# Kernel tuning notes

Hardware: AMD Instinct MI355X
Metric: run time of the kernel (lower is better)

Reference implementation:

```python
import jax, jax.numpy as jnp
import numpy as np

B, C, H, W = 16, 256, 32, 32
NH, DH = 16, 16          # n_heads, n_head_channels; NH*DH == C
STRIDE, KK = 2, 9        # offset conv stride / kernel (stage_idx=0)
Hk, Wk = 16, 16          # offset map size = H/stride
NS = Hk * Wk             # n_sample
EPS_LN, EPS_BN = 1e-5, 1e-5


def conv1x1(x, w, b=None):
    # x: [B,Ci,H,W], w: [Co,Ci]
    y = jnp.einsum('bihw,oi->bohw', x, w)
    if b is not None:
        y = y + b[None, :, None, None]
    return y


def dwconv(x, w, b):
    # depthwise conv, w: [C,1,KK,KK]
    y = jax.lax.conv_general_dilated(
        x, w, (STRIDE, STRIDE), [(KK // 2, KK // 2)] * 2,
        dimension_numbers=('NCHW', 'OIHW', 'NCHW'),
        feature_group_count=x.shape[1])
    return y + b[None, :, None, None]


def ln_channels(x, g, b):
    # LayerNormProxy: layer-norm over channel dim of NCHW
    m = jnp.mean(x, axis=1, keepdims=True)
    v = jnp.mean((x - m) ** 2, axis=1, keepdims=True)
    return (x - m) / jnp.sqrt(v + EPS_LN) * g[None, :, None, None] + b[None, :, None, None]


def ref_points(hk, wk, b):
    # normalized (y, x) reference grid in [-1, 1], matching _get_ref_points
    ry = (jnp.arange(hk, dtype=jnp.float32) + 0.5) / hk * 2.0 - 1.0
    rx = (jnp.arange(wk, dtype=jnp.float32) + 0.5) / wk * 2.0 - 1.0
    ref = jnp.stack(jnp.meshgrid(ry, rx, indexing='ij'), axis=-1)  # [hk,wk,2] (y,x)
    return jnp.broadcast_to(ref[None], (b, hk, wk, 2))


def grid_sample_bilinear(img, grid):
    # img: [B,C,H,W]; grid: [B,Hg,Wg,2] in (x,y) order, [-1,1], align_corners=True,
    # zeros padding (matches torch F.grid_sample defaults).
    Bi, Ci, Hi, Wi = img.shape
    gx = (grid[..., 0] + 1.0) * 0.5 * (Wi - 1)
    gy = (grid[..., 1] + 1.0) * 0.5 * (Hi - 1)
    x0 = jnp.floor(gx); y0 = jnp.floor(gy)
    x1 = x0 + 1.0;      y1 = y0 + 1.0
    wx1 = gx - x0; wx0 = 1.0 - wx1
    wy1 = gy - y0; wy0 = 1.0 - wy1
    imgf = img.reshape(Bi, Ci, Hi * Wi)

    def gather(yi, xi):
        valid = (yi >= 0) & (yi < Hi) & (xi >= 0) & (xi < Wi)
        idx = (jnp.clip(yi, 0, Hi - 1) * Wi + jnp.clip(xi, 0, Wi - 1)).astype(jnp.int32)
        v = jnp.take_along_axis(imgf, idx.reshape(Bi, 1, -1), axis=2)  # [B,C,Hg*Wg]
        return v * valid.reshape(Bi, 1, -1).astype(img.dtype)

    out = (gather(y0, x0) * (wy0 * wx0).reshape(Bi, 1, -1)
           + gather(y0, x1) * (wy0 * wx1).reshape(Bi, 1, -1)
           + gather(y1, x0) * (wy1 * wx0).reshape(Bi, 1, -1)
           + gather(y1, x1) * (wy1 * wx1).reshape(Bi, 1, -1))
    return out.reshape(Bi, Ci, grid.shape[1], grid.shape[2])


def setup_inputs() -> dict:
    key = jax.random.key(0)
    ks = jax.random.split(key, 16)
    s = 0.05
    return {
        'x':        jax.random.normal(ks[0], (B, C, H, W), jnp.float32),
        'wq':       jax.random.normal(ks[1], (C, C), jnp.float32) * s,
        'bq':       jax.random.normal(ks[2], (C,), jnp.float32) * s,
        'off_dw_w': jax.random.normal(ks[3], (C, 1, KK, KK), jnp.float32) * s,
        'off_dw_b': jax.random.normal(ks[4], (C,), jnp.float32) * s,
        'ln_g':     jnp.ones((C,), jnp.float32),
        'ln_b':     jnp.zeros((C,), jnp.float32),
        'off_pw_w': jax.random.normal(ks[5], (2, C), jnp.float32) * s,
        'wk':       jax.random.normal(ks[6], (C, C), jnp.float32) * s,
        'bk':       jax.random.normal(ks[7], (C,), jnp.float32) * s,
        'wv':       jax.random.normal(ks[8], (C, C), jnp.float32) * s,
        'bv':       jax.random.normal(ks[9], (C,), jnp.float32) * s,
        'wo':       jax.random.normal(ks[10], (C, C), jnp.float32) * s,
        'bo':       jax.random.normal(ks[11], (C,), jnp.float32) * s,
        'bn_g':     jnp.ones((C,), jnp.float32),
        'bn_b':     jnp.zeros((C,), jnp.float32),
        'bn_m':     jax.random.normal(ks[12], (C,), jnp.float32) * s,
        'bn_v':     jax.random.uniform(ks[13], (C,), jnp.float32) + 0.5,
    }


def reference(x, wq, bq, off_dw_w, off_dw_b, ln_g, ln_b, off_pw_w,
              wk, bk, wv, bv, wo, bo, bn_g, bn_b, bn_m, bn_v):
    q = conv1x1(x, wq, bq)                                 # [B,C,H,W]
    # offset branch (n_groups=1 so q_off == q)
    off = dwconv(q, off_dw_w, off_dw_b)                    # [B,C,Hk,Wk]
    off = jax.nn.gelu(ln_channels(off, ln_g, ln_b), approximate=False)
    offset = jnp.einsum('bihw,oi->bohw', off, off_pw_w)    # [B,2,Hk,Wk] (y,x)
    offset = jnp.transpose(offset, (0, 2, 3, 1))           # [B,Hk,Wk,2]
    ref = ref_points(Hk, Wk, B)
    pos = jnp.tanh(offset + ref)                           # offset_range_factor[0] < 0 branch
    # deformable sampling: grid takes (x,y)
    xs = grid_sample_bilinear(x, pos[..., ::-1])           # [B,C,Hk,Wk]
    xs = xs.reshape(B, C, 1, NS)
    k = conv1x1(xs, wk, bk).reshape(B * NH, DH, NS)
    v = conv1x1(xs, wv, bv).reshape(B * NH, DH, NS)
    qf = q.reshape(B * NH, DH, H * W)
    attn = jnp.einsum('bcm,bcn->bmn', qf, k) * (DH ** -0.5)  # [B*NH, H*W, NS]
    attn = jax.nn.softmax(attn, axis=2)
    out = jnp.einsum('bmn,bcn->bcm', attn, v).reshape(B, C, H, W)
    y = conv1x1(out, wo, bo)
    # BatchNorm2d in eval mode with running stats
    y = ((y - bn_m[None, :, None, None]) / jnp.sqrt(bn_v[None, :, None, None] + EPS_BN)
         * bn_g[None, :, None, None] + bn_b[None, :, None, None])
    return y
```

## Files before the change

kernel.cpp:

```cpp
#include <hip/hip_runtime.h>
#include <hip/hip_bf16.h>
#include <math.h>

#define BATCH 16
#define CH    256
#define HW    1024
#define NS    256
#define NH    16
#define DH    16

typedef __attribute__((ext_vector_type(8))) short short8v;
typedef __attribute__((ext_vector_type(4))) float float4v;

__device__ __forceinline__ unsigned short f2bf(float f) {
    union { float f; unsigned u; } v; v.f = f;
    unsigned r = v.u + 0x7FFFu + ((v.u >> 16) & 1u);
    return (unsigned short)(r >> 16);
}

__global__ __launch_bounds__(256) void prep_k(
    const float* __restrict__ wq, const float* __restrict__ wk,
    const float* __restrict__ wv, const float* __restrict__ wo,
    unsigned short* __restrict__ Wf,
    const float* __restrict__ x, unsigned short* __restrict__ xT)
{
    int blk = blockIdx.x;
    if (blk < 1024) {
        const float* W;
        switch (blk >> 8) {
            case 0: W = wq; break;
            case 1: W = wk; break;
            case 2: W = wv; break;
            default: W = wo; break;
        }
        int e = (blk & 255) * 256 + threadIdx.x;
        int i = e & 7, l = (e >> 3) & 63, kt = (e >> 9) & 7, ot = e >> 12;
        float v = W[(ot * 16 + (l & 15)) * 256 + kt * 32 + 8 * (l >> 4) + i];
        Wf[(blk >> 8) * 65536 + e] = f2bf(v);
    } else {
        int xb = blk - 1024;
        int b = xb >> 4, pblk = (xb >> 2) & 3, cblk = xb & 3;
        int p = pblk * 256 + threadIdx.x;
        const float* xp = x + (size_t)b * CH * HW + p;
        unsigned short* o = xT + ((size_t)b * HW + p) * CH;
        #pragma unroll
        for (int cc = 0; cc < 64; cc += 8) {
            int c0 = cblk * 64 + cc;
            short8v t;
            #pragma unroll
            for (int i = 0; i < 8; ++i) t[i] = (short)f2bf(xp[(size_t)(c0 + i) * HW]);
            *(short8v*)&o[c0] = t;
        }
    }
}

template<int P, int MODE>
__global__ __launch_bounds__(256) void gemm_k(
    const unsigned short* __restrict__ Wf, const unsigned short* __restrict__ XT,
    const float* __restrict__ bias, const float* __restrict__ bias2,
    float* __restrict__ outF, unsigned short* __restrict__ outB,
    unsigned short* __restrict__ outB2,
    const float* __restrict__ bn_g, const float* __restrict__ bn_b,
    const float* __restrict__ bn_m, const float* __restrict__ bn_v)
{
    const int bz  = blockIdx.z;
    const int b   = (MODE == 1) ? (bz & 15) : bz;
    const int mat = (MODE == 1) ? (bz >> 4) : 0;
    const unsigned short* Wfm = Wf + mat * 65536;

    const int t = threadIdx.x, lane = t & 63, wvi = t >> 6;
    const int g = lane >> 4, col = lane & 15;
    const int o0 = blockIdx.x * 64;
    const int p0 = blockIdx.y * 128 + wvi * 32;
    const unsigned short* xb = XT + ((size_t)b * P + p0) * CH;

    float4v acc[4][2];
    #pragma unroll
    for (int mi = 0; mi < 4; ++mi)
        #pragma unroll
        for (int ni = 0; ni < 2; ++ni) {
            float4v z = {0.f, 0.f, 0.f, 0.f};
            acc[mi][ni] = z;
        }

    #pragma unroll
    for (int kt = 0; kt < 8; ++kt) {
        short8v af[4], bf[2];
        #pragma unroll
        for (int mi = 0; mi < 4; ++mi)
            af[mi] = *(const short8v*)&Wfm[(((((o0 >> 4) + mi) * 8) + kt) * 64 + lane) * 8];
        #pragma unroll
        for (int ni = 0; ni < 2; ++ni)
            bf[ni] = *(const short8v*)&xb[(size_t)(ni * 16 + col) * CH + kt * 32 + 8 * g];
        #pragma unroll
        for (int mi = 0; mi < 4; ++mi)
            #pragma unroll
            for (int ni = 0; ni < 2; ++ni)
                acc[mi][ni] = __builtin_amdgcn_mfma_f32_16x16x32_bf16(
                    af[mi], bf[ni], acc[mi][ni], 0, 0, 0);
    }

    const float* bp = (MODE == 1 && mat == 1) ? bias2 : bias;
    #pragma unroll
    for (int mi = 0; mi < 4; ++mi) {
        const int ob = o0 + mi * 16 + 4 * g;
        float bs[4];
        #pragma unroll
        for (int ii = 0; ii < 4; ++ii) bs[ii] = bp[ob + ii];

        if (MODE == 2) {
            float sc[4], sh[4];
            #pragma unroll
            for (int ii = 0; ii < 4; ++ii) {
                int o = ob + ii;
                float s = bn_g[o] * rsqrtf(bn_v[o] + 1e-5f);
                sc[ii] = s;
                sh[ii] = bn_b[o] - bn_m[o] * s + bs[ii] * s;
            }
            #pragma unroll
            for (int ni = 0; ni < 2; ++ni) {
                int p = p0 + ni * 16 + col;
                #pragma unroll
                for (int ii = 0; ii < 4; ++ii)
                    outF[((size_t)(b * CH + ob + ii)) * P + p] =
                        acc[mi][ni][ii] * sc[ii] + sh[ii];
            }
        } else {
            #pragma unroll
            for (int ni = 0; ni < 2; ++ni) {
                int p = p0 + ni * 16 + col;
                float v0 = acc[mi][ni][0] + bs[0];
                float v1 = acc[mi][ni][1] + bs[1];
                float v2 = acc[mi][ni][2] + bs[2];
                float v3 = acc[mi][ni][3] + bs[3];
                if (MODE == 0) {
                    outF[((size_t)(b * CH + ob + 0)) * P + p] = v0;
                    outF[((size_t)(b * CH + ob + 1)) * P + p] = v1;
                    outF[((size_t)(b * CH + ob + 2)) * P + p] = v2;
                    outF[((size_t)(b * CH + ob + 3)) * P + p] = v3;
                    uint2 w;
                    w.x = (unsigned)f2bf(v0) | ((unsigned)f2bf(v1) << 16);
                    w.y = (unsigned)f2bf(v2) | ((unsigned)f2bf(v3) << 16);
                    *(uint2*)&outB[((size_t)(b * P + p)) * CH + ob] = w;
                } else {
                    if (mat == 0) {
                        uint2 w;
                        w.x = (unsigned)f2bf(v0) | ((unsigned)f2bf(v1) << 16);
                        w.y = (unsigned)f2bf(v2) | ((unsigned)f2bf(v3) << 16);
                        *(uint2*)&outB[((size_t)(b * P + p)) * CH + ob] = w;
                    } else {
                        outB2[((size_t)(b * CH + ob + 0)) * P + p] = f2bf(v0);
                        outB2[((size_t)(b * CH + ob + 1)) * P + p] = f2bf(v1);
                        outB2[((size_t)(b * CH + ob + 2)) * P + p] = f2bf(v2);
                        outB2[((size_t)(b * CH + ob + 3)) * P + p] = f2bf(v3);
                    }
                }
            }
        }
    }
}

__global__ __launch_bounds__(256) void dwconv_k(
    const float* __restrict__ q, const float* __restrict__ w,
    const float* __restrict__ bias, float* __restrict__ off)
{
    int bc = blockIdx.x;
    int c  = bc & (CH - 1);
    __shared__ float plane[HW];
    __shared__ float kw[81];
    int t = threadIdx.x;
    const float* qp = q + (size_t)bc * HW;
    #pragma unroll
    for (int j = t; j < HW; j += 256) plane[j] = qp[j];
    if (t < 81) kw[t] = w[c * 81 + t];
    __syncthreads();
    int hk = t >> 4, wk = t & 15;
    float s = bias[c];
    int yb = hk * 2 - 4, xb = wk * 2 - 4;
    #pragma unroll
    for (int dy = 0; dy < 9; ++dy) {
        int yy = yb + dy;
        if ((unsigned)yy < 32u) {
            #pragma unroll
            for (int dx = 0; dx < 9; ++dx) {
                int xx = xb + dx;
                if ((unsigned)xx < 32u) s += kw[dy * 9 + dx] * plane[yy * 32 + xx];
            }
        }
    }
    off[(size_t)bc * NS + t] = s;
}

__device__ inline void block_reduce2(float& a, float& b, int t, float* sbuf)
{
    #pragma unroll
    for (int o = 32; o > 0; o >>= 1) {
        a += __shfl_down(a, o);
        b += __shfl_down(b, o);
    }
    int w = t >> 6;
    if ((t & 63) == 0) { sbuf[w * 2] = a; sbuf[w * 2 + 1] = b; }
    __syncthreads();
    a = sbuf[0] + sbuf[2] + sbuf[4] + sbuf[6];
    b = sbuf[1] + sbuf[3] + sbuf[5] + sbuf[7];
    __syncthreads();
}

__global__ __launch_bounds__(256) void lngs_k(
    const float* __restrict__ off, const float* __restrict__ ln_g,
    const float* __restrict__ ln_b, const float* __restrict__ pw,
    const float* __restrict__ x, unsigned short* __restrict__ xsT)
{
    __shared__ float sbuf[8];
    int bs = blockIdx.x;
    int b = bs >> 8, s = bs & 255;
    int c = threadIdx.x;
    float v = off[((size_t)(b * CH + c)) * NS + s];
    float a = v, q2 = v * v;
    block_reduce2(a, q2, c, sbuf);
    float mean = a * (1.0f / 256.0f);
    float var  = q2 * (1.0f / 256.0f) - mean * mean;
    float xn = (v - mean) * rsqrtf(var + 1e-5f) * ln_g[c] + ln_b[c];
    float g = 0.5f * xn * (1.0f + erff(xn * 0.70710678118654752f));
    float d0 = g * pw[c];
    float d1 = g * pw[CH + c];
    block_reduce2(d0, d1, c, sbuf);

    int hk = s >> 4, wk = s & 15;
    float ry = ((hk + 0.5f) / 16.0f) * 2.0f - 1.0f;
    float rx = ((wk + 0.5f) / 16.0f) * 2.0f - 1.0f;
    float py = tanhf(d0 + ry);
    float px = tanhf(d1 + rx);

    float gx = (px + 1.0f) * 0.5f * 31.0f;
    float gy = (py + 1.0f) * 0.5f * 31.0f;
    float x0f = floorf(gx), y0f = floorf(gy);
    int ix = (int)x0f, iy = (int)y0f;
    float wx1 = gx - x0f, wx0 = 1.0f - wx1;
    float wy1 = gy - y0f, wy0 = 1.0f - wy1;
    const float* img = x + ((size_t)b * CH + c) * HW;
    float v00 = ((unsigned)iy < 32u && (unsigned)ix < 32u) ? img[iy * 32 + ix] : 0.0f;
    float v01 = ((unsigned)iy < 32u && (unsigned)(ix + 1) < 32u) ? img[iy * 32 + ix + 1] : 0.0f;
    float v10 = ((unsigned)(iy + 1) < 32u && (unsigned)ix < 32u) ? img[(iy + 1) * 32 + ix] : 0.0f;
    float v11 = ((unsigned)(iy + 1) < 32u && (unsigned)(ix + 1) < 32u) ? img[(iy + 1) * 32 + ix + 1] : 0.0f;
    float vv = wy0 * wx0 * v00 + wy0 * wx1 * v01 + wy1 * wx0 * v10 + wy1 * wx1 * v11;
    xsT[(size_t)bs * CH + c] = f2bf(vv);
}

__global__ __launch_bounds__(256) void attn_mfma_k(
    const unsigned short* __restrict__ qT, const unsigned short* __restrict__ kT,
    const unsigned short* __restrict__ vbf, unsigned short* __restrict__ aoT)
{
    const int bh   = blockIdx.x >> 2;
    const int mseg = blockIdx.x & 3;
    const int b = bh >> 4, h = bh & 15;

    __shared__ short Kp[16 * 64 * 8];
    __shared__ short Vsh[16 * 256];
    __shared__ short Ps[4][16 * 32];

    const int tid  = threadIdx.x;
    const int lane = tid & 63;
    const int wvi  = tid >> 6;
    const int col  = lane & 15;
    const int g    = lane >> 4;

    for (int e = tid; e < 512; e += 256) {
        int t = e >> 5, l = e & 31, gg = l >> 4, c = l & 15;
        short8v kk = *(const short8v*)&kT[((size_t)(b * NS + 16 * t + c)) * CH + h * 16 + 8 * gg];
        *(short8v*)&Kp[(t * 64 + l) * 8] = kk;
        short8v z = {0, 0, 0, 0, 0, 0, 0, 0};
        *(short8v*)&Kp[(t * 64 + 32 + l) * 8] = z;
    }
    {
        const unsigned short* Vb = vbf + ((size_t)(b * CH + h * 16)) * NS;
        int d = tid >> 4, n0 = (tid & 15) * 16;
        char* vb = (char*)Vsh;
        #pragma unroll
        for (int hh = 0; hh < 2; ++hh) {
            short8v pk = *(const short8v*)&Vb[(size_t)d * NS + n0 + 8 * hh];
            *(short8v*)(vb + ((d * 512 + (n0 + 8 * hh) * 2) ^ ((d & 7) << 4))) = pk;
        }
    }
    __syncthreads();

    const unsigned short* Qb = qT + (size_t)b * HW * CH + h * 16;
    unsigned short*       Ob = aoT + (size_t)b * HW * CH + h * 16;
    char* pbase = (char*)Ps[wvi];
    char* vbase = (char*)Vsh;

    for (int mt = 0; mt < 4; ++mt) {
        const int m0 = mseg * 256 + wvi * 64 + mt * 16;

        short8v qf = {0, 0, 0, 0, 0, 0, 0, 0};
        if (g < 2)
            qf = *(const short8v*)&Qb[(size_t)(m0 + col) * CH + 8 * g];

        float4v p[16];
        #pragma unroll
        for (int t = 0; t < 16; ++t) {
            short8v kf = *(const short8v*)&Kp[(t * 64 + lane) * 8];
            float4v z = {0.f, 0.f, 0.f, 0.f};
            p[t] = __builtin_amdgcn_mfma_f32_16x16x32_bf16(kf, qf, z, 0, 0, 0);
        }

        float mx = -1e30f;
        #pragma unroll
        for (int t = 0; t < 16; ++t)
            mx = fmaxf(mx, fmaxf(fmaxf(p[t][0], p[t][1]), fmaxf(p[t][2], p[t][3])));
        mx = fmaxf(mx, __shfl_xor(mx, 16));
        mx = fmaxf(mx, __shfl_xor(mx, 32));
        float sum = 0.f;
        #pragma unroll
        for (int t = 0; t < 16; ++t) {
            #pragma unroll
            for (int i = 0; i < 4; ++i) {
                float e = __expf((p[t][i] - mx) * 0.25f);
                p[t][i] = e;
                sum += e;
            }
        }
        sum += __shfl_xor(sum, 16);
        sum += __shfl_xor(sum, 32);
        const float inv = 1.0f / sum;

        float4v acc = {0.f, 0.f, 0.f, 0.f};
        #pragma unroll
        for (int c = 0; c < 8; ++c) {
            #pragma unroll
            for (int pp = 0; pp < 2; ++pp) {
                float4v pv = p[2 * c + pp];
                uint2 wr;
                wr.x = (unsigned)f2bf(pv[0]) | ((unsigned)f2bf(pv[1]) << 16);
                wr.y = (unsigned)f2bf(pv[2]) | ((unsigned)f2bf(pv[3]) << 16);
                *(uint2*)(pbase + ((col * 64 + (16 * pp + 4 * g) * 2) ^ ((col & 7) << 4))) = wr;
            }
            short8v pf = *(const short8v*)(pbase + ((col * 64 + 16 * g) ^ ((col & 7) << 4)));
            short8v vf = *(const short8v*)(vbase + ((col * 512 + 64 * c + 16 * g) ^ ((col & 7) << 4)));
            acc = __builtin_amdgcn_mfma_f32_16x16x32_bf16(vf, pf, acc, 0, 0, 0);
        }

        uint2 w;
        w.x = (unsigned)f2bf(acc[0] * inv) | ((unsigned)f2bf(acc[1] * inv) << 16);
        w.y = (unsigned)f2bf(acc[2] * inv) | ((unsigned)f2bf(acc[3] * inv) << 16);
        *(uint2*)&Ob[(size_t)(m0 + col) * CH + 4 * g] = w;
    }
}

extern "C" void kernel_launch(void* const* d_in, const int* in_sizes, int n_in,
                              void* d_out, int out_size, void* d_ws, size_t ws_size,
                              hipStream_t stream)
{
    const float* x        = (const float*)d_in[0];
    const float* wq       = (const float*)d_in[1];
    const float* bq       = (const float*)d_in[2];
    const float* off_dw_w = (const float*)d_in[3];
    const float* off_dw_b = (const float*)d_in[4];
    const float* ln_g     = (const float*)d_in[5];
    const float* ln_b     = (const float*)d_in[6];
    const float* off_pw_w = (const float*)d_in[7];
    const float* wk       = (const float*)d_in[8];
    const float* bk       = (const float*)d_in[9];
    const float* wv       = (const float*)d_in[10];
    const float* bv       = (const float*)d_in[11];
    const float* wo       = (const float*)d_in[12];
    const float* bo       = (const float*)d_in[13];
    const float* bn_g     = (const float*)d_in[14];
    const float* bn_b     = (const float*)d_in[15];
    const float* bn_m     = (const float*)d_in[16];
    const float* bn_v     = (const float*)d_in[17];

    float* ws  = (float*)d_ws;
    float* q   = ws;
    float* off = q + 4194304;
    unsigned short* us  = (unsigned short*)(off + 1048576);
    unsigned short* Wf  = us;
    unsigned short* xT  = Wf  + 262144;
    unsigned short* qT  = xT  + 4194304;
    unsigned short* xsT = qT  + 4194304;
    unsigned short* kT  = xsT + 1048576;
    unsigned short* vbf = kT  + 1048576;
    unsigned short* aoT = vbf + 1048576;

    prep_k<<<1280, 256, 0, stream>>>(wq, wk, wv, wo, Wf, x, xT);
    gemm_k<HW, 0><<<dim3(4, 8, BATCH), 256, 0, stream>>>(
        Wf, xT, bq, nullptr, q, qT, nullptr, nullptr, nullptr, nullptr, nullptr);
    dwconv_k<<<BATCH * CH, 256, 0, stream>>>(q, off_dw_w, off_dw_b, off);
    lngs_k<<<BATCH * NS, 256, 0, stream>>>(off, ln_g, ln_b, off_pw_w, x, xsT);
    gemm_k<NS, 1><<<dim3(4, 2, 2 * BATCH), 256, 0, stream>>>(
        Wf + 65536, xsT, bk, bv, nullptr, kT, vbf, nullptr, nullptr, nullptr, nullptr);
    attn_mfma_k<<<BATCH * NH * 4, 256, 0, stream>>>(qT, kT, vbf, aoT);
    gemm_k<HW, 2><<<dim3(4, 8, BATCH), 256, 0, stream>>>(
        Wf + 3 * 65536, aoT, bo, nullptr, (float*)d_out, nullptr, nullptr,
        bn_g, bn_b, bn_m, bn_v);
}
```

Before: 119.8 us.

## Fuse x transpose and Q projection into one kernel; transpose offset layout

New measurement: 123.4 us. +3.0%, slower.

```diff
diff --git a/kernel.cpp b/kernel.cpp
--- a/kernel.cpp
+++ b/kernel.cpp
@@ -18,38 +18,105 @@
     return (unsigned short)(r >> 16);
 }
 
-__global__ __launch_bounds__(256) void prep_k(
+__device__ __forceinline__ short8v pack8(float4 a, float4 b) {
+    short8v r;
+    r[0] = (short)f2bf(a.x); r[1] = (short)f2bf(a.y);
+    r[2] = (short)f2bf(a.z); r[3] = (short)f2bf(a.w);
+    r[4] = (short)f2bf(b.x); r[5] = (short)f2bf(b.y);
+    r[6] = (short)f2bf(b.z); r[7] = (short)f2bf(b.w);
+    return r;
+}
+
+__global__ __launch_bounds__(256) void gemmq_k(
     const float* __restrict__ wq, const float* __restrict__ wk,
     const float* __restrict__ wv, const float* __restrict__ wo,
-    unsigned short* __restrict__ Wf,
-    const float* __restrict__ x, unsigned short* __restrict__ xT)
-{
-    int blk = blockIdx.x;
-    if (blk < 1024) {
-        const float* W;
-        switch (blk >> 8) {
-            case 0: W = wq; break;
-            case 1: W = wk; break;
-            case 2: W = wv; break;
-            default: W = wo; break;
-        }
-        int e = (blk & 255) * 256 + threadIdx.x;
-        int i = e & 7, l = (e >> 3) & 63, kt = (e >> 9) & 7, ot = e >> 12;
-        float v = W[(ot * 16 + (l & 15)) * 256 + kt * 32 + 8 * (l >> 4) + i];
-        Wf[(blk >> 8) * 65536 + e] = f2bf(v);
-    } else {
-        int xb = blk - 1024;
-        int b = xb >> 4, pblk = (xb >> 2) & 3, cblk = xb & 3;
-        int p = pblk * 256 + threadIdx.x;
-        const float* xp = x + (size_t)b * CH * HW + p;
-        unsigned short* o = xT + ((size_t)b * HW + p) * CH;
-        #pragma unroll
-        for (int cc = 0; cc < 64; cc += 8) {
-            int c0 = cblk * 64 + cc;
-            short8v t;
-            #pragma unroll
-            for (int i = 0; i < 8; ++i) t[i] = (short)f2bf(xp[(size_t)(c0 + i) * HW]);
-            *(short8v*)&o[c0] = t;
+    const float* __restrict__ x, const float* __restrict__ bias,
+    float* __restrict__ q, unsigned short* __restrict__ qT,
+    unsigned short* __restrict__ Wf)
+{
+    const int blk = blockIdx.x;
+    if (blk >= 512) {
+        int e = (blk - 512) * 256 + threadIdx.x;
+        int mat = e >> 16;
+        int ee = e & 65535;
+        const float* W = (mat == 0) ? wk : (mat == 1) ? wv : wo;
+        int i = ee & 7, l = (ee >> 3) & 63, kt = (ee >> 9) & 7, ot = ee >> 12;
+        Wf[(mat + 1) * 65536 + ee] =
+            f2bf(W[(ot * 16 + (l & 15)) * 256 + kt * 32 + 8 * (l >> 4) + i]);
+        return;
+    }
+
+    const int b  = blk & 15;
+    const int py = (blk >> 4) & 7;
+    const int ox = blk >> 7;
+
+    const int t = threadIdx.x, lane = t & 63, wvi = t >> 6;
+    const int g = lane >> 4, col = lane & 15;
+    const int o0 = ox * 64;
+    const int p0 = py * 128 + wvi * 32;
+    const float* xb = x + (size_t)b * CH * HW;
+
+    float4v acc[4][2];
+    #pragma unroll
+    for (int mi = 0; mi < 4; ++mi)
+        #pragma unroll
+        for (int ni = 0; ni < 2; ++ni) {
+            float4v z = {0.f, 0.f, 0.f, 0.f};
+            acc[mi][ni] = z;
+        }
+
+    #pragma unroll
+    for (int kt = 0; kt < 8; ++kt) {
+        const int kb = kt * 32 + 8 * g;
+        short8v af[4], bf[2];
+        #pragma unroll
+        for (int mi = 0; mi < 4; ++mi) {
+            const float* wp = wq + (size_t)(o0 + mi * 16 + col) * CH + kb;
+            af[mi] = pack8(*(const float4*)wp, *(const float4*)(wp + 4));
+        }
+        #pragma unroll
+        for (int ni = 0; ni < 2; ++ni) {
+            const int p = p0 + ni * 16 + col;
+            float4 lo, hi;
+            lo.x = xb[(size_t)(kb + 0) * HW + p];
+            lo.y = xb[(size_t)(kb + 1) * HW + p];
+            lo.z = xb[(size_t)(kb + 2) * HW + p];
+            lo.w = xb[(size_t)(kb + 3) * HW + p];
+            hi.x = xb[(size_t)(kb + 4) * HW + p];
+            hi.y = xb[(size_t)(kb + 5) * HW + p];
+            hi.z = xb[(size_t)(kb + 6) * HW + p];
+            hi.w = xb[(size_t)(kb + 7) * HW + p];
+            bf[ni] = pack8(lo, hi);
+        }
+        #pragma unroll
+        for (int mi = 0; mi < 4; ++mi)
+            #pragma unroll
+            for (int ni = 0; ni < 2; ++ni)
+                acc[mi][ni] = __builtin_amdgcn_mfma_f32_16x16x32_bf16(
+                    af[mi], bf[ni], acc[mi][ni], 0, 0, 0);
+    }
+
+    #pragma unroll
+    for (int mi = 0; mi < 4; ++mi) {
+        const int ob = o0 + mi * 16 + 4 * g;
+        float bs[4];
+        #pragma unroll
+        for (int ii = 0; ii < 4; ++ii) bs[ii] = bias[ob + ii];
+        #pragma unroll
+        for (int ni = 0; ni < 2; ++ni) {
+            int p = p0 + ni * 16 + col;
+            float v0 = acc[mi][ni][0] + bs[0];
+            float v1 = acc[mi][ni][1] + bs[1];
+            float v2 = acc[mi][ni][2] + bs[2];
+            float v3 = acc[mi][ni][3] + bs[3];
+            q[((size_t)(b * CH + ob + 0)) * HW + p] = v0;
+            q[((size_t)(b * CH + ob + 1)) * HW + p] = v1;
+            q[((size_t)(b * CH + ob + 2)) * HW + p] = v2;
+            q[((size_t)(b * CH + ob + 3)) * HW + p] = v3;
+            uint2 w;
+            w.x = (unsigned)f2bf(v0) | ((unsigned)f2bf(v1) << 16);
+            w.y = (unsigned)f2bf(v2) | ((unsigned)f2bf(v3) << 16);
+            *(uint2*)&qT[((size_t)(b * HW + p)) * CH + ob] = w;
         }
     }
 }
@@ -133,27 +200,16 @@
                 float v1 = acc[mi][ni][1] + bs[1];
                 float v2 = acc[mi][ni][2] + bs[2];
                 float v3 = acc[mi][ni][3] + bs[3];
-                if (MODE == 0) {
-                    outF[((size_t)(b * CH + ob + 0)) * P + p] = v0;
-                    outF[((size_t)(b * CH + ob + 1)) * P + p] = v1;
-                    outF[((size_t)(b * CH + ob + 2)) * P + p] = v2;
-                    outF[((size_t)(b * CH + ob + 3)) * P + p] = v3;
+                if (mat == 0) {
                     uint2 w;
                     w.x = (unsigned)f2bf(v0) | ((unsigned)f2bf(v1) << 16);
                     w.y = (unsigned)f2bf(v2) | ((unsigned)f2bf(v3) << 16);
                     *(uint2*)&outB[((size_t)(b * P + p)) * CH + ob] = w;
                 } else {
-                    if (mat == 0) {
-                        uint2 w;
-                        w.x = (unsigned)f2bf(v0) | ((unsigned)f2bf(v1) << 16);
-                        w.y = (unsigned)f2bf(v2) | ((unsigned)f2bf(v3) << 16);
-                        *(uint2*)&outB[((size_t)(b * P + p)) * CH + ob] = w;
-                    } else {
-                        outB2[((size_t)(b * CH + ob + 0)) * P + p] = f2bf(v0);
-                        outB2[((size_t)(b * CH + ob + 1)) * P + p] = f2bf(v1);
-                        outB2[((size_t)(b * CH + ob + 2)) * P + p] = f2bf(v2);
-                        outB2[((size_t)(b * CH + ob + 3)) * P + p] = f2bf(v3);
-                    }
+                    outB2[((size_t)(b * CH + ob + 0)) * P + p] = f2bf(v0);
+                    outB2[((size_t)(b * CH + ob + 1)) * P + p] = f2bf(v1);
+                    outB2[((size_t)(b * CH + ob + 2)) * P + p] = f2bf(v2);
+                    outB2[((size_t)(b * CH + ob + 3)) * P + p] = f2bf(v3);
                 }
             }
         }
@@ -162,9 +218,10 @@
 
 __global__ __launch_bounds__(256) void dwconv_k(
     const float* __restrict__ q, const float* __restrict__ w,
-    const float* __restrict__ bias, float* __restrict__ off)
+    const float* __restrict__ bias, float* __restrict__ offT)
 {
     int bc = blockIdx.x;
+    int b  = bc >> 8;
     int c  = bc & (CH - 1);
     __shared__ float plane[HW];
     __shared__ float kw[81];
@@ -188,7 +245,7 @@
             }
         }
     }
-    off[(size_t)bc * NS + t] = s;
+    offT[((size_t)(b * NS + t)) * CH + c] = s;
 }
 
 __device__ inline void block_reduce2(float& a, float& b, int t, float* sbuf)
@@ -207,7 +264,7 @@
 }
 
 __global__ __launch_bounds__(256) void lngs_k(
-    const float* __restrict__ off, const float* __restrict__ ln_g,
+    const float* __restrict__ offT, const float* __restrict__ ln_g,
     const float* __restrict__ ln_b, const float* __restrict__ pw,
     const float* __restrict__ x, unsigned short* __restrict__ xsT)
 {
@@ -215,7 +272,7 @@
     int bs = blockIdx.x;
     int b = bs >> 8, s = bs & 255;
     int c = threadIdx.x;
-    float v = off[((size_t)(b * CH + c)) * NS + s];
+    float v = offT[(size_t)bs * CH + c];
     float a = v, q2 = v * v;
     block_reduce2(a, q2, c, sbuf);
     float mean = a * (1.0f / 256.0f);
@@ -370,23 +427,20 @@
     const float* bn_m     = (const float*)d_in[16];
     const float* bn_v     = (const float*)d_in[17];
 
-    float* ws  = (float*)d_ws;
-    float* q   = ws;
-    float* off = q + 4194304;
-    unsigned short* us  = (unsigned short*)(off + 1048576);
+    float* ws   = (float*)d_ws;
+    float* q    = ws;
+    float* offT = q + 4194304;
+    unsigned short* us  = (unsigned short*)(offT + 1048576);
     unsigned short* Wf  = us;
-    unsigned short* xT  = Wf  + 262144;
-    unsigned short* qT  = xT  + 4194304;
+    unsigned short* qT  = Wf  + 262144;
     unsigned short* xsT = qT  + 4194304;
     unsigned short* kT  = xsT + 1048576;
     unsigned short* vbf = kT  + 1048576;
     unsigned short* aoT = vbf + 1048576;
 
-    prep_k<<<1280, 256, 0, stream>>>(wq, wk, wv, wo, Wf, x, xT);
-    gemm_k<HW, 0><<<dim3(4, 8, BATCH), 256, 0, stream>>>(
-        Wf, xT, bq, nullptr, q, qT, nullptr, nullptr, nullptr, nullptr, nullptr);
-    dwconv_k<<<BATCH * CH, 256, 0, stream>>>(q, off_dw_w, off_dw_b, off);
-    lngs_k<<<BATCH * NS, 256, 0, stream>>>(off, ln_g, ln_b, off_pw_w, x, xsT);
+    gemmq_k<<<1280, 256, 0, stream>>>(wq, wk, wv, wo, x, bq, q, qT, Wf);
+    dwconv_k<<<BATCH * CH, 256, 0, stream>>>(q, off_dw_w, off_dw_b, offT);
+    lngs_k<<<BATCH * NS, 256, 0, stream>>>(offT, ln_g, ln_b, off_pw_w, x, xsT);
     gemm_k<NS, 1><<<dim3(4, 2, 2 * BATCH), 256, 0, stream>>>(
         Wf + 65536, xsT, bk, bv, nullptr, kT, vbf, nullptr, nullptr, nullptr, nullptr);
     attn_mfma_k<<<BATCH * NH * 4, 256, 0, stream>>>(qT, kT, vbf, aoT);
```

## Fuse K/V projection GEMM into attention kernel prologue

Applied to the files above, without the earlier changes.

After: 121.9 us. Within noise of the previous version (+1.8%).

```diff
diff --git a/kernel.cpp b/kernel.cpp
--- a/kernel.cpp
+++ b/kernel.cpp
@@ -57,16 +57,12 @@
 template<int P, int MODE>
 __global__ __launch_bounds__(256) void gemm_k(
     const unsigned short* __restrict__ Wf, const unsigned short* __restrict__ XT,
-    const float* __restrict__ bias, const float* __restrict__ bias2,
+    const float* __restrict__ bias,
     float* __restrict__ outF, unsigned short* __restrict__ outB,
-    unsigned short* __restrict__ outB2,
     const float* __restrict__ bn_g, const float* __restrict__ bn_b,
     const float* __restrict__ bn_m, const float* __restrict__ bn_v)
 {
-    const int bz  = blockIdx.z;
-    const int b   = (MODE == 1) ? (bz & 15) : bz;
-    const int mat = (MODE == 1) ? (bz >> 4) : 0;
-    const unsigned short* Wfm = Wf + mat * 65536;
+    const int b = blockIdx.z;
 
     const int t = threadIdx.x, lane = t & 63, wvi = t >> 6;
     const int g = lane >> 4, col = lane & 15;
@@ -88,7 +84,7 @@
         short8v af[4], bf[2];
         #pragma unroll
         for (int mi = 0; mi < 4; ++mi)
-            af[mi] = *(const short8v*)&Wfm[(((((o0 >> 4) + mi) * 8) + kt) * 64 + lane) * 8];
+            af[mi] = *(const short8v*)&Wf[(((((o0 >> 4) + mi) * 8) + kt) * 64 + lane) * 8];
         #pragma unroll
         for (int ni = 0; ni < 2; ++ni)
             bf[ni] = *(const short8v*)&xb[(size_t)(ni * 16 + col) * CH + kt * 32 + 8 * g];
@@ -100,13 +96,12 @@
                     af[mi], bf[ni], acc[mi][ni], 0, 0, 0);
     }
 
-    const float* bp = (MODE == 1 && mat == 1) ? bias2 : bias;
     #pragma unroll
     for (int mi = 0; mi < 4; ++mi) {
         const int ob = o0 + mi * 16 + 4 * g;
         float bs[4];
         #pragma unroll
-        for (int ii = 0; ii < 4; ++ii) bs[ii] = bp[ob + ii];
+        for (int ii = 0; ii < 4; ++ii) bs[ii] = bias[ob + ii];
 
         if (MODE == 2) {
             float sc[4], sh[4];
@@ -133,28 +128,14 @@
                 float v1 = acc[mi][ni][1] + bs[1];
                 float v2 = acc[mi][ni][2] + bs[2];
                 float v3 = acc[mi][ni][3] + bs[3];
-                if (MODE == 0) {
-                    outF[((size_t)(b * CH + ob + 0)) * P + p] = v0;
-                    outF[((size_t)(b * CH + ob + 1)) * P + p] = v1;
-                    outF[((size_t)(b * CH + ob + 2)) * P + p] = v2;
-                    outF[((size_t)(b * CH + ob + 3)) * P + p] = v3;
-                    uint2 w;
-                    w.x = (unsigned)f2bf(v0) | ((unsigned)f2bf(v1) << 16);
-                    w.y = (unsigned)f2bf(v2) | ((unsigned)f2bf(v3) << 16);
-                    *(uint2*)&outB[((size_t)(b * P + p)) * CH + ob] = w;
-                } else {
-                    if (mat == 0) {
-                        uint2 w;
-                        w.x = (unsigned)f2bf(v0) | ((unsigned)f2bf(v1) << 16);
-                        w.y = (unsigned)f2bf(v2) | ((unsigned)f2bf(v3) << 16);
-                        *(uint2*)&outB[((size_t)(b * P + p)) * CH + ob] = w;
-                    } else {
-                        outB2[((size_t)(b * CH + ob + 0)) * P + p] = f2bf(v0);
-                        outB2[((size_t)(b * CH + ob + 1)) * P + p] = f2bf(v1);
-                        outB2[((size_t)(b * CH + ob + 2)) * P + p] = f2bf(v2);
-                        outB2[((size_t)(b * CH + ob + 3)) * P + p] = f2bf(v3);
-                    }
-                }
+                outF[((size_t)(b * CH + ob + 0)) * P + p] = v0;
+                outF[((size_t)(b * CH + ob + 1)) * P + p] = v1;
+                outF[((size_t)(b * CH + ob + 2)) * P + p] = v2;
+                outF[((size_t)(b * CH + ob + 3)) * P + p] = v3;
+                uint2 w;
+                w.x = (unsigned)f2bf(v0) | ((unsigned)f2bf(v1) << 16);
+                w.y = (unsigned)f2bf(v2) | ((unsigned)f2bf(v3) << 16);
+                *(uint2*)&outB[((size_t)(b * P + p)) * CH + ob] = w;
             }
         }
     }
@@ -247,16 +228,18 @@
     xsT[(size_t)bs * CH + c] = f2bf(vv);
 }
 
-__global__ __launch_bounds__(256) void attn_mfma_k(
-    const unsigned short* __restrict__ qT, const unsigned short* __restrict__ kT,
-    const unsigned short* __restrict__ vbf, unsigned short* __restrict__ aoT)
+__global__ __launch_bounds__(256) void attn_fused_k(
+    const unsigned short* __restrict__ qT, const unsigned short* __restrict__ xsT,
+    const unsigned short* __restrict__ Wf,
+    const float* __restrict__ bk, const float* __restrict__ bv,
+    unsigned short* __restrict__ aoT)
 {
     const int bh   = blockIdx.x >> 2;
     const int mseg = blockIdx.x & 3;
     const int b = bh >> 4, h = bh & 15;
 
     __shared__ short Kp[16 * 64 * 8];
-    __shared__ short Vsh[16 * 256];
+    __shared__ short Vp[8 * 64 * 8];
     __shared__ short Ps[4][16 * 32];
 
     const int tid  = threadIdx.x;
@@ -265,21 +248,42 @@
     const int col  = lane & 15;
     const int g    = lane >> 4;
 
-    for (int e = tid; e < 512; e += 256) {
-        int t = e >> 5, l = e & 31, gg = l >> 4, c = l & 15;
-        short8v kk = *(const short8v*)&kT[((size_t)(b * NS + 16 * t + c)) * CH + h * 16 + 8 * gg];
-        *(short8v*)&Kp[(t * 64 + l) * 8] = kk;
+    {
+        const unsigned short* WfK = Wf + 1 * 65536 + h * 4096;
+        const unsigned short* WfV = Wf + 2 * 65536 + h * 4096;
+        float bk4[4];
+        #pragma unroll
+        for (int j = 0; j < 4; ++j) bk4[j] = bk[h * 16 + 4 * g + j];
+        const float bvv = bv[h * 16 + col];
+
+        #pragma unroll
+        for (int tt = 0; tt < 4; ++tt) {
+            const int t  = wvi * 4 + tt;
+            const int n0 = t * 16;
+            float4v accK = {0.f, 0.f, 0.f, 0.f};
+            float4v accV = {0.f, 0.f, 0.f, 0.f};
+            #pragma unroll
+            for (int kt = 0; kt < 8; ++kt) {
+                short8v xsf = *(const short8v*)&xsT[((size_t)(b * NS + n0 + col)) * CH + kt * 32 + 8 * g];
+                short8v wkf = *(const short8v*)&WfK[(kt * 64 + lane) * 8];
+                short8v wvf = *(const short8v*)&WfV[(kt * 64 + lane) * 8];
+                accK = __builtin_amdgcn_mfma_f32_16x16x32_bf16(wkf, xsf, accK, 0, 0, 0);
+                accV = __builtin_amdgcn_mfma_f32_16x16x32_bf16(xsf, wvf, accV, 0, 0, 0);
+            }
+            uint2 wrk;
+            wrk.x = (unsigned)f2bf(accK[0] + bk4[0]) | ((unsigned)f2bf(accK[1] + bk4[1]) << 16);
+            wrk.y = (unsigned)f2bf(accK[2] + bk4[2]) | ((unsigned)f2bf(accK[3] + bk4[3]) << 16);
+            *(uint2*)&Kp[(t * 64 + (g >> 1) * 16 + col) * 8 + 4 * (g & 1)] = wrk;
+            uint2 wrv;
+            wrv.x = (unsigned)f2bf(accV[0] + bvv) | ((unsigned)f2bf(accV[1] + bvv) << 16);
+            wrv.y = (unsigned)f2bf(accV[2] + bvv) | ((unsigned)f2bf(accV[3] + bvv) << 16);
+            *(uint2*)&Vp[((t >> 1) * 64 + col + 16 * ((2 * t + (g >> 1)) & 3)) * 8 + 4 * (g & 1)] = wrv;
+        }
         short8v z = {0, 0, 0, 0, 0, 0, 0, 0};
-        *(short8v*)&Kp[(t * 64 + 32 + l) * 8] = z;
-    }
-    {
-        const unsigned short* Vb = vbf + ((size_t)(b * CH + h * 16)) * NS;
-        int d = tid >> 4, n0 = (tid & 15) * 16;
-        char* vb = (char*)Vsh;
-        #pragma unroll
-        for (int hh = 0; hh < 2; ++hh) {
-            short8v pk = *(const short8v*)&Vb[(size_t)d * NS + n0 + 8 * hh];
-            *(short8v*)(vb + ((d * 512 + (n0 + 8 * hh) * 2) ^ ((d & 7) << 4))) = pk;
+        #pragma unroll
+        for (int e = tid; e < 512; e += 256) {
+            int t = e >> 5, l = e & 31;
+            *(short8v*)&Kp[(t * 64 + 32 + l) * 8] = z;
         }
     }
     __syncthreads();
@@ -287,7 +291,6 @@
     const unsigned short* Qb = qT + (size_t)b * HW * CH + h * 16;
     unsigned short*       Ob = aoT + (size_t)b * HW * CH + h * 16;
     char* pbase = (char*)Ps[wvi];
-    char* vbase = (char*)Vsh;
 
     for (int mt = 0; mt < 4; ++mt) {
         const int m0 = mseg * 256 + wvi * 64 + mt * 16;
@@ -336,7 +339,7 @@
                 *(uint2*)(pbase + ((col * 64 + (16 * pp + 4 * g) * 2) ^ ((col & 7) << 4))) = wr;
             }
             short8v pf = *(const short8v*)(pbase + ((col * 64 + 16 * g) ^ ((col & 7) << 4)));
-            short8v vf = *(const short8v*)(vbase + ((col * 512 + 64 * c + 16 * g) ^ ((col & 7) << 4)));
+            short8v vf = *(const short8v*)&Vp[(c * 64 + lane) * 8];
             acc = __builtin_amdgcn_mfma_f32_16x16x32_bf16(vf, pf, acc, 0, 0, 0);
         }
 
@@ -378,19 +381,15 @@
     unsigned short* xT  = Wf  + 262144;
     unsigned short* qT  = xT  + 4194304;
     unsigned short* xsT = qT  + 4194304;
-    unsigned short* kT  = xsT + 1048576;
-    unsigned short* vbf = kT  + 1048576;
-    unsigned short* aoT = vbf + 1048576;
+    unsigned short* aoT = xsT + 1048576;
 
     prep_k<<<1280, 256, 0, stream>>>(wq, wk, wv, wo, Wf, x, xT);
     gemm_k<HW, 0><<<dim3(4, 8, BATCH), 256, 0, stream>>>(
-        Wf, xT, bq, nullptr, q, qT, nullptr, nullptr, nullptr, nullptr, nullptr);
+        Wf, xT, bq, q, qT, nullptr, nullptr, nullptr, nullptr);
     dwconv_k<<<BATCH * CH, 256, 0, stream>>>(q, off_dw_w, off_dw_b, off);
     lngs_k<<<BATCH * NS, 256, 0, stream>>>(off, ln_g, ln_b, off_pw_w, x, xsT);
-    gemm_k<NS, 1><<<dim3(4, 2, 2 * BATCH), 256, 0, stream>>>(
-        Wf + 65536, xsT, bk, bv, nullptr, kT, vbf, nullptr, nullptr, nullptr, nullptr);
-    attn_mfma_k<<<BATCH * NH * 4, 256, 0, stream>>>(qT, kT, vbf, aoT);
+    attn_fused_k<<<BATCH * NH * 4, 256, 0, stream>>>(qT, xsT, Wf, bk, bv, aoT);
     gemm_k<HW, 2><<<dim3(4, 8, BATCH), 256, 0, stream>>>(
-        Wf + 3 * 65536, aoT, bo, nullptr, (float*)d_out, nullptr, nullptr,
+        Wf + 3 * 65536, aoT, bo, (float*)d_out, nullptr,
         bn_g, bn_b, bn_m, bn_v);
 }
```
